# Performance work log

Hardware: AMD Instinct MI355X
Metric: run time of the kernel (lower is better)

## Reference

```python
import jax, jax.numpy as jnp
import numpy as np

H = 16
D_MODEL = 1024
D_K = D_MODEL // H
WINDOW = 50
ROPE_BASE = 10000.0


def _rope_tables(seq_len, dim, dtype):
    inv_freq = 1.0 / (ROPE_BASE ** (jnp.arange(0, dim, 2, dtype=jnp.float32) / dim))
    t = jnp.arange(seq_len, dtype=jnp.float32)
    freqs = t[:, None] * inv_freq[None, :]          # [S, dim/2]
    emb = jnp.concatenate([freqs, freqs], axis=-1)  # [S, dim]
    return jnp.cos(emb).astype(dtype), jnp.sin(emb).astype(dtype)


def _rotate_half(x):
    d = x.shape[-1] // 2
    return jnp.concatenate([-x[..., d:], x[..., :d]], axis=-1)


def setup_inputs() -> dict:
    key = jax.random.key(0)
    ks = jax.random.split(key, 11)
    B, S = 2, 2048
    scale = 1.0 / np.sqrt(D_MODEL)
    inp = {
        'query': jax.random.normal(ks[0], (B, S, D_MODEL), jnp.float32),
        'key':   jax.random.normal(ks[1], (B, S, D_MODEL), jnp.float32),
        'value': jax.random.normal(ks[2], (B, S, D_MODEL), jnp.float32),
        'Wq': jax.random.normal(ks[3], (D_MODEL, D_MODEL), jnp.float32) * scale,
        'bq': jnp.zeros((D_MODEL,), jnp.float32),
        'Wk': jax.random.normal(ks[4], (D_MODEL, D_MODEL), jnp.float32) * scale,
        'bk': jnp.zeros((D_MODEL,), jnp.float32),
        'Wv': jax.random.normal(ks[5], (D_MODEL, D_MODEL), jnp.float32) * scale,
        'bv': jnp.zeros((D_MODEL,), jnp.float32),
        'Wo': jax.random.normal(ks[6], (D_MODEL, D_MODEL), jnp.float32) * scale,
        'bo': jnp.zeros((D_MODEL,), jnp.float32),
    }
    return inp


def reference(query, key, value, Wq, bq, Wk, bk, Wv, bv, Wo, bo):
    B, S, _ = query.shape
    # QKV projections (torch Linear: x @ W.T + b), split into heads -> [B,H,S,Dk]
    def proj(x, W, b):
        return (x @ W.T + b).reshape(B, S, H, D_K).transpose(0, 2, 1, 3)
    q = proj(query, Wq, bq)
    k = proj(key, Wk, bk)
    v = proj(value, Wv, bv)

    cos, sin = _rope_tables(S, D_K, q.dtype)  # [S, Dk]
    q = q * cos + _rotate_half(q) * sin
    k = k * cos + _rotate_half(k) * sin

    scores = jnp.einsum('bhqd,bhkd->bhqk', q, k) / np.sqrt(D_K)
    # sliding-window mask: |i-j| <= WINDOW
    idx = jnp.arange(S)
    dist = jnp.abs(idx[None, :] - idx[:, None])  # [S, S]
    scores = jnp.where(dist <= WINDOW, scores, jnp.asarray(-1e9, scores.dtype))

    p = jax.nn.softmax(scores, axis=-1)
    out = jnp.einsum('bhqk,bhkd->bhqd', p, v)          # [B,H,S,Dk]
    out = out.transpose(0, 2, 1, 3).reshape(B, S, D_MODEL)
    return out @ Wo.T + bo
```

## Files before the change

kernel.cpp:

```cpp
#include <hip/hip_runtime.h>
#include <hip/hip_bf16.h>
#include <math.h>

typedef __bf16 bf16_t;
typedef __bf16 bf16x8 __attribute__((ext_vector_type(8)));
typedef float floatx4 __attribute__((ext_vector_type(4)));
typedef unsigned int u32;
typedef unsigned short u16;
typedef unsigned long long u64;

#define NHEAD 16

__device__ __forceinline__ void gload_lds16(const void* g, void* l) {
    __builtin_amdgcn_global_load_lds((const __attribute__((address_space(1))) u32*)g,
                                     (__attribute__((address_space(3))) u32*)l, 16, 0, 0);
}

__device__ __forceinline__ u32 pack2(float x, float y) {
    bf16_t a = (bf16_t)x, b = (bf16_t)y;
    return (u32)*(u16*)&a | ((u32)*(u16*)&b << 16);
}

__global__ __launch_bounds__(256) void k_prep(
    const float* __restrict__ q, const float* __restrict__ k, const float* __restrict__ v,
    const float* __restrict__ wq, const float* __restrict__ wk,
    const float* __restrict__ wv, const float* __restrict__ wo,
    bf16_t* __restrict__ Xq, bf16_t* __restrict__ Xk, bf16_t* __restrict__ Xv,
    bf16_t* __restrict__ Wqb, bf16_t* __restrict__ Wkb, bf16_t* __restrict__ Wvb,
    bf16_t* __restrict__ Wob, float* __restrict__ ct, float* __restrict__ st)
{
    int b = blockIdx.x;
    if (b < 8192) {
        const float* src; bf16_t* dst; int off;
        if      (b < 2048) { src = q;  dst = Xq;  off = b; }
        else if (b < 4096) { src = k;  dst = Xk;  off = b - 2048; }
        else if (b < 6144) { src = v;  dst = Xv;  off = b - 4096; }
        else if (b < 6656) { src = wq; dst = Wqb; off = b - 6144; }
        else if (b < 7168) { src = wk; dst = Wkb; off = b - 6656; }
        else if (b < 7680) { src = wv; dst = Wvb; off = b - 7168; }
        else               { src = wo; dst = Wob; off = b - 7680; }
        int i = (off * 256 + threadIdx.x) * 8;
        float4 a = *(const float4*)(src + i);
        float4 c = *(const float4*)(src + i + 4);
        bf16x8 o;
        o[0]=(bf16_t)a.x; o[1]=(bf16_t)a.y; o[2]=(bf16_t)a.z; o[3]=(bf16_t)a.w;
        o[4]=(bf16_t)c.x; o[5]=(bf16_t)c.y; o[6]=(bf16_t)c.z; o[7]=(bf16_t)c.w;
        *(bf16x8*)(dst + i) = o;
    } else {
        int idx = (b - 8192) * 256 + threadIdx.x;
        int s = idx >> 5, i = idx & 31;
        float e = (float)(2 * i) / 64.0f;
        float invf = 1.0f / powf(10000.0f, e);
        float ang = (float)s * invf;
        ct[idx] = cosf(ang);
        st[idx] = sinf(ang);
    }
}

__global__ __launch_bounds__(256,3) void k_gemm_qkv(
    const bf16_t* __restrict__ Xq, const bf16_t* __restrict__ Xk, const bf16_t* __restrict__ Xv,
    const bf16_t* __restrict__ Wqb, const bf16_t* __restrict__ Wkb, const bf16_t* __restrict__ Wvb,
    const float* __restrict__ bq, const float* __restrict__ bk, const float* __restrict__ bv,
    bf16_t* __restrict__ Qr, bf16_t* __restrict__ Kr, bf16_t* __restrict__ Vh,
    const float* __restrict__ ct, const float* __restrict__ st)
{
    __shared__ __align__(16) bf16_t As[2][4096];
    __shared__ __align__(16) bf16_t Bs[2][4096];

    int b0 = blockIdx.x;
    int wg = (b0 & 7) * 96 + (b0 >> 3);
    int id  = wg >> 8;
    int bid = wg & 255;

    const bf16_t* A   = (id==0) ? Xq  : (id==1) ? Xk  : Xv;
    const bf16_t* Wt  = (id==0) ? Wqb : (id==1) ? Wkb : Wvb;
    const float*  bias= (id==0) ? bq  : (id==1) ? bk  : bv;
    bf16_t* out = (id==0) ? Qr : (id==1) ? Kr : Vh;
    bool do_rope = (id < 2);

    int bm = (bid >> 3) << 7;
    int bn = (bid & 7) << 7;
    int tid = threadIdx.x;
    int l = tid & 63, wid = tid >> 6;
    int wr = wid >> 1, wc = wid & 1;
    int fr = l & 15, kg = l >> 4;

    floatx4 acc[4][4];
    #pragma unroll
    for (int i = 0; i < 4; ++i)
        #pragma unroll
        for (int j = 0; j < 4; ++j) acc[i][j] = (floatx4){0.f,0.f,0.f,0.f};

    int srow = tid >> 2;
    int scol = ((tid & 3) ^ (srow & 3)) << 3;
    const bf16_t* Ap0 = A  + ((size_t)(bm + srow) << 10) + scol;
    const bf16_t* Ap1 = A  + ((size_t)(bm + 64 + srow) << 10) + scol;
    const bf16_t* Bp0 = Wt + ((size_t)(bn + srow) << 10) + scol;
    const bf16_t* Bp1 = Wt + ((size_t)(bn + 64 + srow) << 10) + scol;

    gload_lds16(Ap0, &As[0][tid << 3]);
    gload_lds16(Ap1, &As[0][(tid + 256) << 3]);
    gload_lds16(Bp0, &Bs[0][tid << 3]);
    gload_lds16(Bp1, &Bs[0][(tid + 256) << 3]);
    __syncthreads();

    int a_off = fr * 64 + ((kg ^ (fr & 3)) << 4);
    int cur = 0;
    for (int t = 0; t < 32; ++t) {
        if (t < 31) {
            int k0 = (t + 1) << 5;
            gload_lds16(Ap0 + k0, &As[cur ^ 1][tid << 3]);
            gload_lds16(Ap1 + k0, &As[cur ^ 1][(tid + 256) << 3]);
            gload_lds16(Bp0 + k0, &Bs[cur ^ 1][tid << 3]);
            gload_lds16(Bp1 + k0, &Bs[cur ^ 1][(tid + 256) << 3]);
        }
        bf16x8 af[4], bfr[4];
        #pragma unroll
        for (int i = 0; i < 4; ++i)
            af[i]  = *(const bf16x8*)((const char*)As[cur] + (((wr << 2) + i) << 10) + a_off);
        #pragma unroll
        for (int j = 0; j < 4; ++j)
            bfr[j] = *(const bf16x8*)((const char*)Bs[cur] + (((wc << 2) + j) << 10) + a_off);
        #pragma unroll
        for (int i = 0; i < 4; ++i)
            #pragma unroll
            for (int j = 0; j < 4; ++j)
                acc[i][j] = __builtin_amdgcn_mfma_f32_16x16x32_bf16(af[i], bfr[j], acc[i][j], 0, 0, 0);
        __syncthreads();
        cur ^= 1;
    }

    int h = (bn + (wc<<6)) >> 6;
    #pragma unroll
    for (int i = 0; i < 4; ++i) {
        #pragma unroll
        for (int r = 0; r < 4; ++r) {
            int m  = bm + (wr<<6) + (i<<4) + (kg<<2) + r;
            int b_ = m >> 11, s_ = m & 2047;
            size_t ob = ((((size_t)(b_*NHEAD + h)) << 11) + s_) << 6;
            if (do_rope) {
                #pragma unroll
                for (int j = 0; j < 2; ++j) {
                    int d = (j<<4) + fr;
                    float lo = acc[i][j][r]   + bias[bn + (wc<<6) + d];
                    float hv = acc[i][j+2][r] + bias[bn + (wc<<6) + d + 32];
                    float c = ct[(s_<<5) + d], sn = st[(s_<<5) + d];
                    out[ob + d]      = (bf16_t)(lo*c - hv*sn);
                    out[ob + d + 32] = (bf16_t)(hv*c + lo*sn);
                }
            } else {
                #pragma unroll
                for (int j = 0; j < 4; ++j) {
                    int d = (j<<4) + fr;
                    out[ob + d] = (bf16_t)(acc[i][j][r] + bias[bn + (wc<<6) + d]);
                }
            }
        }
    }
}

__global__ __launch_bounds__(256,4) void k_gemm_o(
    const bf16_t* __restrict__ A, const bf16_t* __restrict__ Wt,
    const float* __restrict__ bias, float* __restrict__ out)
{
    __shared__ __align__(16) bf16_t As[2][2048];
    __shared__ __align__(16) bf16_t Bs[2][2048];

    int b0 = blockIdx.x;
    int wg = (b0 & 7) * 128 + (b0 >> 3);
    int bm = (wg >> 4) << 6;
    int bn = (wg & 15) << 6;
    int tid = threadIdx.x;
    int l = tid & 63, wid = tid >> 6;
    int fr = l & 15, kg = l >> 4;

    floatx4 acc[4];
    #pragma unroll
    for (int j = 0; j < 4; ++j) acc[j] = (floatx4){0.f,0.f,0.f,0.f};

    int srow = tid >> 2;
    int scol = ((tid & 3) ^ (srow & 3)) << 3;
    const bf16_t* Ap = A  + ((size_t)(bm + srow) << 10) + scol;
    const bf16_t* Bp = Wt + ((size_t)(bn + srow) << 10) + scol;

    gload_lds16(Ap, &As[0][tid << 3]);
    gload_lds16(Bp, &Bs[0][tid << 3]);
    __syncthreads();

    int a_off = fr * 64 + ((kg ^ (fr & 3)) << 4);
    int cur = 0;
    for (int t = 0; t < 32; ++t) {
        if (t < 31) {
            int k0 = (t + 1) << 5;
            gload_lds16(Ap + k0, &As[cur ^ 1][tid << 3]);
            gload_lds16(Bp + k0, &Bs[cur ^ 1][tid << 3]);
        }
        bf16x8 af, bfr[4];
        af = *(const bf16x8*)((const char*)As[cur] + (wid << 10) + a_off);
        #pragma unroll
        for (int j = 0; j < 4; ++j)
            bfr[j] = *(const bf16x8*)((const char*)Bs[cur] + (j << 10) + a_off);
        #pragma unroll
        for (int j = 0; j < 4; ++j)
            acc[j] = __builtin_amdgcn_mfma_f32_16x16x32_bf16(af, bfr[j], acc[j], 0, 0, 0);
        __syncthreads();
        cur ^= 1;
    }

    #pragma unroll
    for (int r = 0; r < 4; ++r) {
        int m = bm + (wid << 4) + (kg << 2) + r;
        #pragma unroll
        for (int j = 0; j < 4; ++j) {
            int n = bn + (j << 4) + fr;
            out[((size_t)m << 10) + n] = acc[j][r] + bias[n];
        }
    }
}

__global__ __launch_bounds__(256,3) void k_attn(
    const bf16_t* __restrict__ Qr, const bf16_t* __restrict__ Kr,
    const bf16_t* __restrict__ Vh, bf16_t* __restrict__ AO)
{
    __shared__ char smem[51200];
    char* VtB  = smem;
    char* Pall = smem + 25600;

    int q0 = blockIdx.x << 6;
    int h = blockIdx.y, b_ = blockIdx.z;
    int kstart = q0 - 64; if (kstart < 0) kstart = 0;
    int kend   = q0 + 128; if (kend > 2048) kend = 2048;
    int NR = kend - kstart;

    int tid = threadIdx.x, l = tid & 63, w = tid >> 6;
    int q16 = l & 15, g = l >> 4, hi8 = g << 3;

    const bf16_t* Kbase = Kr + (((((size_t)(b_*NHEAD + h)) << 11) + kstart) << 6);
    const bf16_t* Vbase = Vh + (((((size_t)(b_*NHEAD + h)) << 11) + kstart) << 6);

    #pragma unroll
    for (int it = 0; it < 6; ++it) {
        int c = tid + (it << 8);
        int jd2 = c >> 4;
        int dq  = (c & 15) << 2;
        int j0 = jd2 << 1, j1 = j0 + 1;
        int j0c = j0 < NR ? j0 : NR - 1;
        int j1c = j1 < NR ? j1 : NR - 1;
        ushort4 v0 = *(const ushort4*)(Vbase + (j0c << 6) + dq);
        ushort4 v1 = *(const ushort4*)(Vbase + (j1c << 6) + dq);
        u16 a0[4] = {(u16)v0.x,(u16)v0.y,(u16)v0.z,(u16)v0.w};
        u16 a1[4] = {(u16)v1.x,(u16)v1.y,(u16)v1.z,(u16)v1.w};
        #pragma unroll
        for (int t = 0; t < 4; ++t) {
            int d = dq + t;
            u32 pair = (u32)a0[t] | ((u32)a1[t] << 16);
            *(u32*)(VtB + d * 400 + ((jd2 << 2) ^ (((d >> 3) & 7) << 4))) = pair;
        }
    }

    int qs = q0 + (w << 4) + q16;
    const bf16_t* Qbase = Qr + (((((size_t)(b_*NHEAD + h)) << 11) + qs) << 6);
    bf16x8 qf0 = *(const bf16x8*)(Qbase + hi8);
    bf16x8 qf1 = *(const bf16x8*)(Qbase + 32 + hi8);

    floatx4 sc[12];
    __builtin_amdgcn_s_setprio(1);
    #pragma unroll
    for (int kt = 0; kt < 12; ++kt) {
        int krow = (kt << 4) + q16;
        int krc = krow < NR ? krow : NR - 1;
        bf16x8 kf0 = *(const bf16x8*)(Kbase + (krc << 6) + hi8);
        bf16x8 kf1 = *(const bf16x8*)(Kbase + (krc << 6) + 32 + hi8);
        floatx4 a = (floatx4){0.f,0.f,0.f,0.f};
        a = __builtin_amdgcn_mfma_f32_16x16x32_bf16(kf0, qf0, a, 0, 0, 0);
        a = __builtin_amdgcn_mfma_f32_16x16x32_bf16(kf1, qf1, a, 0, 0, 0);
        sc[kt] = a;
    }
    __builtin_amdgcn_s_setprio(0);

    int qrow = q0 + (w << 4) + q16;
    float mx = -1e30f;
    #pragma unroll
    for (int kt = 0; kt < 12; ++kt)
        #pragma unroll
        for (int r = 0; r < 4; ++r) {
            int key = kstart + (kt << 4) + (g << 2) + r;
            int dd = qrow - key; dd = dd < 0 ? -dd : dd;
            float sv = sc[kt][r] * 0.125f;
            sv = (dd <= 50 && key < kend) ? sv : -1e30f;
            sc[kt][r] = sv;
            mx = fmaxf(mx, sv);
        }
    mx = fmaxf(mx, __shfl_xor(mx, 16));
    mx = fmaxf(mx, __shfl_xor(mx, 32));
    float sum = 0.f;
    #pragma unroll
    for (int kt = 0; kt < 12; ++kt)
        #pragma unroll
        for (int r = 0; r < 4; ++r) {
            float p = __expf(sc[kt][r] - mx);
            sc[kt][r] = p;
            sum += p;
        }
    sum += __shfl_xor(sum, 16);
    sum += __shfl_xor(sum, 32);
    float inv = 1.0f / sum;

    char* PwB = Pall + w * 6400;
    int swz = (q16 & 7) << 4;
    #pragma unroll
    for (int t = 0; t < 12; ++t) {
        u32 lo = pack2(sc[t][0] * inv, sc[t][1] * inv);
        u32 hi = pack2(sc[t][2] * inv, sc[t][3] * inv);
        *(u64*)(PwB + q16 * 400 + (((t << 5) + (g << 3)) ^ swz)) = (u64)lo | ((u64)hi << 32);
    }

    __syncthreads();

    floatx4 oc[4];
    #pragma unroll
    for (int dt = 0; dt < 4; ++dt) oc[dt] = (floatx4){0.f,0.f,0.f,0.f};
    __builtin_amdgcn_s_setprio(1);
    #pragma unroll
    for (int kc = 0; kc < 6; ++kc) {
        int keyoff = (kc << 6) + (g << 4);
        bf16x8 pf = *(const bf16x8*)(PwB + q16 * 400 + (keyoff ^ swz));
        #pragma unroll
        for (int dt = 0; dt < 4; ++dt) {
            int d = (dt << 4) + q16;
            bf16x8 vf = *(const bf16x8*)(VtB + d * 400 + (keyoff ^ (((d >> 3) & 7) << 4)));
            oc[dt] = __builtin_amdgcn_mfma_f32_16x16x32_bf16(vf, pf, oc[dt], 0, 0, 0);
        }
    }
    __builtin_amdgcn_s_setprio(0);

    asm volatile("s_waitcnt lgkmcnt(0)" ::: "memory");
    __builtin_amdgcn_sched_barrier(0);
    #pragma unroll
    for (int dt = 0; dt < 4; ++dt)
        #pragma unroll
        for (int r = 0; r < 4; ++r) {
            int d = (dt << 4) + (g << 2) + r;
            *(bf16_t*)(PwB + q16 * 400 + (d << 1)) = (bf16_t)oc[dt][r];
        }
    asm volatile("s_waitcnt lgkmcnt(0)" ::: "memory");
    __builtin_amdgcn_sched_barrier(0);
    #pragma unroll
    for (int it = 0; it < 2; ++it) {
        int c = l + (it << 6);
        int row = c >> 3, off = (c & 7) << 4;
        bf16x8 ov = *(const bf16x8*)(PwB + row * 400 + off);
        int q_abs = q0 + (w << 4) + row;
        *(bf16x8*)(AO + (((size_t)(b_ * 2048 + q_abs)) << 10) + (h << 6) + ((c & 7) << 3)) = ov;
    }
}

extern "C" void kernel_launch(void* const* d_in, const int* in_sizes, int n_in,
                              void* d_out, int out_size, void* d_ws, size_t ws_size,
                              hipStream_t stream)
{
    const float* query = (const float*)d_in[0];
    const float* key_  = (const float*)d_in[1];
    const float* value = (const float*)d_in[2];
    const float* Wq = (const float*)d_in[3];
    const float* bq = (const float*)d_in[4];
    const float* Wk = (const float*)d_in[5];
    const float* bk = (const float*)d_in[6];
    const float* Wv = (const float*)d_in[7];
    const float* bv = (const float*)d_in[8];
    const float* Wo = (const float*)d_in[9];
    const float* bo = (const float*)d_in[10];

    char* ws = (char*)d_ws;
    bf16_t* Xq  = (bf16_t*)(ws);
    bf16_t* Xk  = (bf16_t*)(ws + 8388608);
    bf16_t* Xv  = (bf16_t*)(ws + 16777216);
    bf16_t* Wqb = (bf16_t*)(ws + 25165824);
    bf16_t* Wkb = (bf16_t*)(ws + 27262976);
    bf16_t* Wvb = (bf16_t*)(ws + 29360128);
    bf16_t* Wob = (bf16_t*)(ws + 31457280);
    bf16_t* Qr  = (bf16_t*)(ws + 33554432);
    bf16_t* Kr  = (bf16_t*)(ws + 41943040);
    bf16_t* Vh  = (bf16_t*)(ws + 50331648);
    bf16_t* AO  = (bf16_t*)(ws + 58720256);
    float*  ct  = (float*)(ws + 67108864);
    float*  st  = (float*)(ws + 67371008);

    k_prep<<<8448, 256, 0, stream>>>(query, key_, value, Wq, Wk, Wv, Wo,
                                     Xq, Xk, Xv, Wqb, Wkb, Wvb, Wob, ct, st);
    k_gemm_qkv<<<768, 256, 0, stream>>>(Xq, Xk, Xv, Wqb, Wkb, Wvb,
                                        bq, bk, bv, Qr, Kr, Vh, ct, st);
    k_attn<<<dim3(32, 16, 2), 256, 0, stream>>>(Qr, Kr, Vh, AO);
    k_gemm_o<<<1024, 256, 0, stream>>>(AO, Wob, bo, (float*)d_out);
}
```

Baseline: 103.1 us.

## Stage K tile in LDS via async global_load_lds and write attention output directly

K rows for the window are now copied into a swizzled LDS buffer with async global-to-LDS loads, replacing per-wave direct global loads of K fragments. The P buffer reuses the K region after a second barrier. The PV MFMA operand order is swapped so each lane holds output by query row, and results are stored straight to global as scalar bf16 instead of being staged through LDS for vectorized 16-byte writes. setprio hints are removed. The change cuts redundant global K reads across waves, at the cost of an extra block barrier and narrower, less coalesced output stores.

```diff
diff --git a/kernel.cpp b/kernel.cpp
--- a/kernel.cpp
+++ b/kernel.cpp
@@ -223,8 +223,8 @@
     const bf16_t* __restrict__ Vh, bf16_t* __restrict__ AO)
 {
     __shared__ char smem[51200];
-    char* VtB  = smem;
-    char* Pall = smem + 25600;
+    char* KsPs = smem;
+    char* VtB  = smem + 25600;
 
     int q0 = blockIdx.x << 6;
     int h = blockIdx.y, b_ = blockIdx.z;
@@ -238,6 +238,15 @@
     const bf16_t* Kbase = Kr + (((((size_t)(b_*NHEAD + h)) << 11) + kstart) << 6);
     const bf16_t* Vbase = Vh + (((((size_t)(b_*NHEAD + h)) << 11) + kstart) << 6);
 
+    #pragma unroll
+    for (int it = 0; it < 6; ++it) {
+        int c = tid + (it << 8);
+        int y = c << 4;
+        int row = y >> 7, oz = y & 127;
+        int srw = row < NR ? row : NR - 1;
+        int src = (srw << 7) + (oz ^ ((row & 7) << 4));
+        gload_lds16((const char*)Kbase + src, KsPs + y);
+    }
     #pragma unroll
     for (int it = 0; it < 6; ++it) {
         int c = tid + (it << 8);
@@ -257,26 +266,26 @@
             *(u32*)(VtB + d * 400 + ((jd2 << 2) ^ (((d >> 3) & 7) << 4))) = pair;
         }
     }
-
     int qs = q0 + (w << 4) + q16;
     const bf16_t* Qbase = Qr + (((((size_t)(b_*NHEAD + h)) << 11) + qs) << 6);
     bf16x8 qf0 = *(const bf16x8*)(Qbase + hi8);
     bf16x8 qf1 = *(const bf16x8*)(Qbase + 32 + hi8);
 
+    __syncthreads();
+
     floatx4 sc[12];
-    __builtin_amdgcn_s_setprio(1);
     #pragma unroll
     for (int kt = 0; kt < 12; ++kt) {
-        int krow = (kt << 4) + q16;
-        int krc = krow < NR ? krow : NR - 1;
-        bf16x8 kf0 = *(const bf16x8*)(Kbase + (krc << 6) + hi8);
-        bf16x8 kf1 = *(const bf16x8*)(Kbase + (krc << 6) + 32 + hi8);
+        int row = (kt << 4) + q16;
+        int base = (row << 7) + (hi8 << 1);
+        int swzk = (row & 7) << 4;
+        bf16x8 kf0 = *(const bf16x8*)(KsPs + (base ^ swzk));
+        bf16x8 kf1 = *(const bf16x8*)(KsPs + ((base + 64) ^ swzk));
         floatx4 a = (floatx4){0.f,0.f,0.f,0.f};
         a = __builtin_amdgcn_mfma_f32_16x16x32_bf16(kf0, qf0, a, 0, 0, 0);
         a = __builtin_amdgcn_mfma_f32_16x16x32_bf16(kf1, qf1, a, 0, 0, 0);
         sc[kt] = a;
     }
-    __builtin_amdgcn_s_setprio(0);
 
     int qrow = q0 + (w << 4) + q16;
     float mx = -1e30f;
@@ -306,53 +315,38 @@
     sum += __shfl_xor(sum, 32);
     float inv = 1.0f / sum;
 
-    char* PwB = Pall + w * 6400;
+    __syncthreads();
+
+    char* PwB = KsPs + w * 6400;
     int swz = (q16 & 7) << 4;
     #pragma unroll
-    for (int t = 0; t < 12; ++t) {
-        u32 lo = pack2(sc[t][0] * inv, sc[t][1] * inv);
-        u32 hi = pack2(sc[t][2] * inv, sc[t][3] * inv);
-        *(u64*)(PwB + q16 * 400 + (((t << 5) + (g << 3)) ^ swz)) = (u64)lo | ((u64)hi << 32);
-    }
-
-    __syncthreads();
+    for (int kt = 0; kt < 12; ++kt) {
+        u32 lo = pack2(sc[kt][0] * inv, sc[kt][1] * inv);
+        u32 hi = pack2(sc[kt][2] * inv, sc[kt][3] * inv);
+        *(u64*)(PwB + q16 * 400 + (((kt << 5) + (g << 3)) ^ swz)) = (u64)lo | ((u64)hi << 32);
+    }
 
     floatx4 oc[4];
     #pragma unroll
     for (int dt = 0; dt < 4; ++dt) oc[dt] = (floatx4){0.f,0.f,0.f,0.f};
-    __builtin_amdgcn_s_setprio(1);
-    #pragma unroll
-    for (int kc = 0; kc < 6; ++kc) {
-        int keyoff = (kc << 6) + (g << 4);
+    #pragma unroll
+    for (int ks = 0; ks < 6; ++ks) {
+        int keyoff = (ks << 6) + (g << 4);
         bf16x8 pf = *(const bf16x8*)(PwB + q16 * 400 + (keyoff ^ swz));
         #pragma unroll
         for (int dt = 0; dt < 4; ++dt) {
             int d = (dt << 4) + q16;
             bf16x8 vf = *(const bf16x8*)(VtB + d * 400 + (keyoff ^ (((d >> 3) & 7) << 4)));
-            oc[dt] = __builtin_amdgcn_mfma_f32_16x16x32_bf16(vf, pf, oc[dt], 0, 0, 0);
-        }
-    }
-    __builtin_amdgcn_s_setprio(0);
-
-    asm volatile("s_waitcnt lgkmcnt(0)" ::: "memory");
-    __builtin_amdgcn_sched_barrier(0);
+            oc[dt] = __builtin_amdgcn_mfma_f32_16x16x32_bf16(pf, vf, oc[dt], 0, 0, 0);
+        }
+    }
     #pragma unroll
     for (int dt = 0; dt < 4; ++dt)
         #pragma unroll
         for (int r = 0; r < 4; ++r) {
-            int d = (dt << 4) + (g << 2) + r;
-            *(bf16_t*)(PwB + q16 * 400 + (d << 1)) = (bf16_t)oc[dt][r];
-        }
-    asm volatile("s_waitcnt lgkmcnt(0)" ::: "memory");
-    __builtin_amdgcn_sched_barrier(0);
-    #pragma unroll
-    for (int it = 0; it < 2; ++it) {
-        int c = l + (it << 6);
-        int row = c >> 3, off = (c & 7) << 4;
-        bf16x8 ov = *(const bf16x8*)(PwB + row * 400 + off);
-        int q_abs = q0 + (w << 4) + row;
-        *(bf16x8*)(AO + (((size_t)(b_ * 2048 + q_abs)) << 10) + (h << 6) + ((c & 7) << 3)) = ov;
-    }
+            int qq = q0 + (w << 4) + (g << 2) + r;
+            AO[(((size_t)(b_ * 2048 + qq)) << 10) + (h << 6) + (dt << 4) + q16] = (bf16_t)oc[dt][r];
+        }
 }
 
 extern "C" void kernel_launch(void* const* d_in, const int* in_sizes, int n_in,
```

Result: faster. 94.89 us (-7.9%).
